# Kernel tuning notes

Hardware: AMD Instinct MI355X
Metric: run time of the kernel (lower is better)

Reference implementation:

```python
import jax, jax.numpy as jnp
import numpy as np
from jax import lax

# ---- module config (init_kwargs) ----
B, CIN, COUT, H, W, K = 16, 32, 32, 256, 256, 3
FEATURE_BITS = 8
INPUT_ZP = 3
OUTPUT_ZP = -5
INPUT_SCALE = 0.02
OUTPUT_SCALE = 0.05
STRIDE = (1, 1)
PAD_H, PAD_W = 1, 1
DILATION = (1, 1)
GROUPS = 1
QMIN, QMAX = -(2 ** (FEATURE_BITS - 1)), 2 ** (FEATURE_BITS - 1) - 1  # -128, 127


def float_to_fixed_point(scale, bitwidth):
    # Represent scale (in (0,1)) as int_scale * 2^-frac_bits with int_scale <= 2^(b-1)-1.
    # Pick the largest frac_bits s.t. round(scale * 2^frac_bits) fits -> max precision.
    qmax = jnp.float32(2 ** (bitwidth - 1) - 1)
    frac_bits = jnp.floor(jnp.log2(qmax / scale)).astype(jnp.int32)
    int_scale = jnp.round(scale * jnp.exp2(frac_bits.astype(jnp.float32))).astype(jnp.int32)
    return int_scale, frac_bits


def setup_inputs() -> dict:
    key = jax.random.key(0)
    k0, k1, k2, k3 = jax.random.split(key, 4)
    x = jax.random.randint(k0, (B, CIN, H, W), -128, 128, dtype=jnp.int32).astype(jnp.int8)
    qweight = jax.random.randint(k1, (COUT, CIN, K, K), -128, 128, dtype=jnp.int32).astype(jnp.int8)
    qbias = jax.random.randint(k2, (COUT,), -1000, 1000, dtype=jnp.int32)
    weight_scale = jax.random.uniform(k3, (COUT,), jnp.float32, 1e-3, 1e-2)
    return {"x": x, "qweight": qweight, "qbias": qbias, "weight_scale": weight_scale}


def reference(x, qweight, qbias, weight_scale):
    # F.pad(qinput, (pw,pw,ph,ph), 'constant', input_zero_point) -> pad W and H dims
    xp = jnp.pad(x, ((0, 0), (0, 0), (PAD_H, PAD_H), (PAD_W, PAD_W)),
                 mode="constant", constant_values=INPUT_ZP)
    # int32 conv (no bias), VALID since input was pre-padded
    out = lax.conv_general_dilated(
        xp.astype(jnp.int32), qweight.astype(jnp.int32),
        window_strides=STRIDE, padding="VALID", rhs_dilation=DILATION,
        dimension_numbers=("NCHW", "OIHW", "NCHW"), feature_group_count=GROUPS)
    # shifted bias: qbias - sum(qweight) * input_zero_point  (per out channel)
    shifted_qbias = qbias - qweight.astype(jnp.int32).sum((1, 2, 3)) * INPUT_ZP
    out = out + shifted_qbias[None, :, None, None]
    # fixed-point requant: (out * int_scale) >> frac_bits, per channel
    folded_scale = (INPUT_SCALE * weight_scale / OUTPUT_SCALE).astype(jnp.float32)
    int_scale, frac_bits = float_to_fixed_point(folded_scale, FEATURE_BITS)
    out = jnp.right_shift(out * int_scale[None, :, None, None],
                          frac_bits[None, :, None, None])  # arithmetic shift on int32
    out = out + OUTPUT_ZP
    out = jnp.clip(out, QMIN, QMAX).astype(jnp.int8)
    return out
```

## Files before the change

### kernel.cpp

```cpp
#include <hip/hip_runtime.h>

#define B_   16
#define CIN  32
#define COUT 32
#define H_   256
#define W_   256
#define IN_ZP  3
#define OUT_ZP (-5)
#define TH 4
#define TW 64
#define HW (H_ * W_)

#if defined(__has_builtin)
#if __has_builtin(__builtin_amdgcn_sdot4)
#define HAVE_SDOT4 1
#endif
#endif

__device__ __forceinline__ int dot4(int a, int b, int c) {
#ifdef HAVE_SDOT4
    return __builtin_amdgcn_sdot4(a, b, c, false);
#else
    c += ((a << 24) >> 24) * ((b << 24) >> 24);
    c += ((a << 16) >> 24) * ((b << 16) >> 24);
    c += ((a << 8)  >> 24) * ((b << 8)  >> 24);
    c += (a >> 24) * (b >> 24);
    return c;
#endif
}

__global__ void qconv_prep(const int* __restrict__ qw, const int* __restrict__ qb,
                           const float* __restrict__ wscale, int* __restrict__ ws) {
    int tid = threadIdx.x;
    for (int idx = tid; idx < COUT * 8 * 9; idx += blockDim.x) {
        int co = idx / 72, rem = idx % 72;
        int cig = rem / 9, k = rem % 9;
        int base = co * (CIN * 9) + (cig * 4) * 9 + k;
        int b0 = qw[base]      & 0xff;
        int b1 = qw[base + 9]  & 0xff;
        int b2 = qw[base + 18] & 0xff;
        int b3 = qw[base + 27] & 0xff;
        ws[idx] = b0 | (b1 << 8) | (b2 << 16) | (b3 << 24);
    }
    if (tid < COUT) {
        int co = tid;
        int wsum = 0;
        for (int i = 0; i < CIN * 9; ++i) wsum += qw[co * (CIN * 9) + i];
        int sb = qb[co] - wsum * IN_ZP;
        float fs = (0.02f * wscale[co]) / 0.05f;
        float fb = floorf(log2f(127.0f / fs));
        int frac = (int)fb;
        int iscale = (int)rintf(fs * exp2f(fb));
        ws[2304 + co] = sb;
        ws[2336 + co] = iscale;
        ws[2368 + co] = frac;
    }
}

__global__ __launch_bounds__(256, 2) void qconv_main(const int* __restrict__ x,
                                                     const int* __restrict__ ws,
                                                     int* __restrict__ out) {
    __shared__ int smem[8][TH + 2][TW + 2];
    const int wt = blockIdx.x * TW;
    const int ht = blockIdx.y * TH;
    const int b  = blockIdx.z;
    const int tid = threadIdx.x;
    const int* xb = x + b * (CIN * HW);

    for (int idx = tid; idx < 8 * (TH + 2) * (TW + 2); idx += 256) {
        int cig = idx / ((TH + 2) * (TW + 2));
        int rem = idx % ((TH + 2) * (TW + 2));
        int r = rem / (TW + 2), c = rem % (TW + 2);
        int gh = ht - 1 + r, gw = wt - 1 + c;
        int packed;
        if ((unsigned)gh < H_ && (unsigned)gw < W_) {
            const int* p = xb + (cig * 4) * HW + gh * W_ + gw;
            int v0 = p[0]      & 0xff;
            int v1 = p[HW]     & 0xff;
            int v2 = p[2 * HW] & 0xff;
            int v3 = p[3 * HW] & 0xff;
            packed = v0 | (v1 << 8) | (v2 << 16) | (v3 << 24);
        } else {
            packed = 0x03030303;
        }
        ((int*)smem)[idx] = packed;
    }
    __syncthreads();

    const int row = tid >> 6, col = tid & 63;
    int xr[8][3][3];
#pragma unroll
    for (int cig = 0; cig < 8; ++cig)
#pragma unroll
        for (int r = 0; r < 3; ++r)
#pragma unroll
            for (int c = 0; c < 3; ++c)
                xr[cig][r][c] = smem[cig][row + r][col + c];

    const int* wq  = ws;
    const int* sb  = ws + 2304;
    const int* isc = ws + 2336;
    const int* fbp = ws + 2368;
    int* outp = out + ((b * COUT) * H_ + (ht + row)) * W_ + wt + col;

#pragma unroll 2
    for (int co = 0; co < COUT; ++co) {
        int acc = sb[co];
        const int* w = wq + co * 72;
#pragma unroll
        for (int cig = 0; cig < 8; ++cig) {
#pragma unroll
            for (int k = 0; k < 9; ++k)
                acc = dot4(xr[cig][k / 3][k % 3], w[cig * 9 + k], acc);
        }
        int t = (acc * isc[co]) >> fbp[co];
        t += OUT_ZP;
        t = min(127, max(-128, t));
        outp[co * HW] = t;
    }
}

extern "C" void kernel_launch(void* const* d_in, const int* in_sizes, int n_in,
                              void* d_out, int out_size, void* d_ws, size_t ws_size,
                              hipStream_t stream) {
    const int*   x   = (const int*)d_in[0];
    const int*   qw  = (const int*)d_in[1];
    const int*   qb  = (const int*)d_in[2];
    const float* wsc = (const float*)d_in[3];
    int* ws  = (int*)d_ws;
    int* out = (int*)d_out;

    qconv_prep<<<1, 256, 0, stream>>>(qw, qb, wsc, ws);
    dim3 grid(W_ / TW, H_ / TH, B_);
    qconv_main<<<grid, 256, 0, stream>>>(x, ws, out);
}
```

Before: 290.8 us.

## Swap conv loop order to keep all output-channel accumulators in registers

The main kernel now holds 32 output-channel accumulators per thread and streams one input-channel group of 9 packed pixels at a time, instead of caching all 72 packed inputs in registers and looping over output channels. Weights are re-laid out as [cig*9+k][co] so each tap's weights across channels are contiguous and can be fetched as wide scalar loads. The prep kernel is parallelized across 32 blocks with a wavefront-shuffle reduction for the weight sums, replacing the single-block serial loop. The aim is lower register pressure and better weight-load batching, at the cost of keeping the accumulator array live through the whole loop.

```diff
diff --git a/kernel.cpp b/kernel.cpp
--- a/kernel.cpp
+++ b/kernel.cpp
@@ -31,29 +31,33 @@
 
 __global__ void qconv_prep(const int* __restrict__ qw, const int* __restrict__ qb,
                            const float* __restrict__ wscale, int* __restrict__ ws) {
-    int tid = threadIdx.x;
-    for (int idx = tid; idx < COUT * 8 * 9; idx += blockDim.x) {
-        int co = idx / 72, rem = idx % 72;
-        int cig = rem / 9, k = rem % 9;
+    const int co  = blockIdx.x;
+    const int tid = threadIdx.x;
+    __shared__ int red[4];
+    const int* wco = qw + co * (CIN * 9);
+
+    int s = 0;
+    for (int i = tid; i < CIN * 9; i += 256) s += wco[i];
+    for (int off = 32; off; off >>= 1) s += __shfl_down(s, off, 64);
+    if ((tid & 63) == 0) red[tid >> 6] = s;
+
+    if (tid < 72) {
+        int cig = tid / 9, k = tid % 9;
         int base = co * (CIN * 9) + (cig * 4) * 9 + k;
         int b0 = qw[base]      & 0xff;
         int b1 = qw[base + 9]  & 0xff;
         int b2 = qw[base + 18] & 0xff;
         int b3 = qw[base + 27] & 0xff;
-        ws[idx] = b0 | (b1 << 8) | (b2 << 16) | (b3 << 24);
+        ws[tid * 32 + co] = b0 | (b1 << 8) | (b2 << 16) | (b3 << 24);
     }
-    if (tid < COUT) {
-        int co = tid;
-        int wsum = 0;
-        for (int i = 0; i < CIN * 9; ++i) wsum += qw[co * (CIN * 9) + i];
-        int sb = qb[co] - wsum * IN_ZP;
+    __syncthreads();
+    if (tid == 0) {
+        int wsum = red[0] + red[1] + red[2] + red[3];
+        ws[2304 + co] = qb[co] - wsum * IN_ZP;
         float fs = (0.02f * wscale[co]) / 0.05f;
         float fb = floorf(log2f(127.0f / fs));
-        int frac = (int)fb;
-        int iscale = (int)rintf(fs * exp2f(fb));
-        ws[2304 + co] = sb;
-        ws[2336 + co] = iscale;
-        ws[2368 + co] = frac;
+        ws[2336 + co] = (int)rintf(fs * exp2f(fb));
+        ws[2368 + co] = (int)fb;
     }
 }
 
@@ -88,32 +92,35 @@
     __syncthreads();
 
     const int row = tid >> 6, col = tid & 63;
-    int xr[8][3][3];
+
+    int acc[COUT];
+    const int* sb = ws + 2304;
 #pragma unroll
-    for (int cig = 0; cig < 8; ++cig)
+    for (int co = 0; co < COUT; ++co) acc[co] = sb[co];
+
+#pragma unroll
+    for (int cig = 0; cig < 8; ++cig) {
+        int xv[9];
 #pragma unroll
         for (int r = 0; r < 3; ++r)
 #pragma unroll
             for (int c = 0; c < 3; ++c)
-                xr[cig][r][c] = smem[cig][row + r][col + c];
+                xv[r * 3 + c] = smem[cig][row + r][col + c];
+#pragma unroll
+        for (int k = 0; k < 9; ++k) {
+            const int* w = ws + (cig * 9 + k) * 32;
+#pragma unroll
+            for (int co = 0; co < COUT; ++co)
+                acc[co] = dot4(xv[k], w[co], acc[co]);
+        }
+    }
 
-    const int* wq  = ws;
-    const int* sb  = ws + 2304;
     const int* isc = ws + 2336;
     const int* fbp = ws + 2368;
     int* outp = out + ((b * COUT) * H_ + (ht + row)) * W_ + wt + col;
-
-#pragma unroll 2
+#pragma unroll
     for (int co = 0; co < COUT; ++co) {
-        int acc = sb[co];
-        const int* w = wq + co * 72;
-#pragma unroll
-        for (int cig = 0; cig < 8; ++cig) {
-#pragma unroll
-            for (int k = 0; k < 9; ++k)
-                acc = dot4(xr[cig][k / 3][k % 3], w[cig * 9 + k], acc);
-        }
-        int t = (acc * isc[co]) >> fbp[co];
+        int t = (acc[co] * isc[co]) >> fbp[co];
         t += OUT_ZP;
         t = min(127, max(-128, t));
         outp[co * HW] = t;
@@ -130,7 +137,7 @@
     int* ws  = (int*)d_ws;
     int* out = (int*)d_out;
 
-    qconv_prep<<<1, 256, 0, stream>>>(qw, qb, wsc, ws);
+    qconv_prep<<<32, 256, 0, stream>>>(qw, qb, wsc, ws);
     dim3 grid(W_ / TW, H_ / TH, B_);
     qconv_main<<<grid, 256, 0, stream>>>(x, ws, out);
 }
```

Result: no change. 289.8 us (-0.3%).
